# Performance work log

Hardware: AMD Instinct MI355X
Metric: run time of the kernel (lower is better)

The kernel has to match this reference:

```python
import math
import jax, jax.numpy as jnp
from jax import lax
import numpy as np

DT = 1.0 / 252.0  # dt_anos (dt_dias=1)

def _mlp(x, W1, b1, W2, b2, W3, b3):
    h = jax.nn.gelu(x @ W1 + b1, approximate=False)
    h = jax.nn.gelu(h @ W2 + b2, approximate=False)
    return h @ W3 + b3

def setup_inputs() -> dict:
    key = jax.random.key(0)
    ks = jax.random.split(key, 20)
    B, T = 64, 256
    d_ctx, d_h = 64 * 3, 128
    d_in = d_ctx + 2  # [r_mean, t_norm, ctx]
    def lin(k, din, dout):
        return jax.random.normal(k, (din, dout), dtype=jnp.float32) / np.sqrt(din)
    inp = {
        "X": jax.random.normal(ks[0], (B, T, 2), dtype=jnp.float32),
        "r_ultimo": jax.random.uniform(ks[1], (B,), dtype=jnp.float32) * 0.1,
        "maturidades": jnp.array([0.25, 0.5, 1.0, 2.0, 3.0, 5.0, 10.0], dtype=jnp.float32),
        "Wp": lin(ks[2], 2, 64), "bp": jnp.zeros((64,), jnp.float32),
        "ln_g": jnp.ones((64,), jnp.float32), "ln_b": jnp.zeros((64,), jnp.float32),
        "mu_W1": lin(ks[3], d_in, d_h), "mu_b1": jnp.zeros((d_h,), jnp.float32),
        "mu_W2": lin(ks[4], d_h, d_h), "mu_b2": jnp.zeros((d_h,), jnp.float32),
        "mu_W3": lin(ks[5], d_h, 1), "mu_b3": jnp.zeros((1,), jnp.float32),
        "si_W1": lin(ks[6], d_in, d_h), "si_b1": jnp.zeros((d_h,), jnp.float32),
        "si_W2": lin(ks[7], d_h, d_h), "si_b2": jnp.zeros((d_h,), jnp.float32),
        "si_W3": lin(ks[8], d_h, 1), "si_b3": jnp.zeros((1,), jnp.float32),
    }
    return inp

def _forward(n_steps, X, r_ultimo, maturidades, Wp, bp, ln_g, ln_b,
             mu_W1, mu_b1, mu_W2, mu_b2, mu_W3, mu_b3,
             si_W1, si_b1, si_W2, si_b2, si_W3, si_b3, Q=256):
    B = X.shape[0]
    # --- AgregadorContexto: LN(tanh(Linear(X))), mean/std(unbiased)/last ---
    H = jnp.tanh(X @ Wp + bp)                       # (B,T,64)
    m = H.mean(-1, keepdims=True)
    v = ((H - m) ** 2).mean(-1, keepdims=True)
    H = (H - m) / jnp.sqrt(v + 1e-5) * ln_g + ln_b
    ctx = jnp.concatenate([H.mean(1), H.std(1, ddof=1), H[:, -1, :]], axis=1)  # (B,192)
    # --- Euler-Maruyama MC of neural SDE ---
    max_T = maturidades.max()
    t_grid = jnp.linspace(0.0, 1.0, n_steps)
    keys = jax.random.split(jax.random.key(1), n_steps)
    sqrt_dt = math.sqrt(DT)
    def step(carry, inp):
        r, area = carry                              # (B,Q)
        t, k = inp
        x = jnp.concatenate(
            [r.mean(1, keepdims=True), jnp.broadcast_to(t, (B, 1)), ctx], axis=1)  # (B,194)
        mu = _mlp(x, mu_W1, mu_b1, mu_W2, mu_b2, mu_W3, mu_b3)[:, 0]
        si = jax.nn.softplus(_mlp(x, si_W1, si_b1, si_W2, si_b2, si_W3, si_b3)[:, 0]) + 1e-5
        dW = jax.random.normal(k, r.shape, dtype=r.dtype) * sqrt_dt
        r = r + mu[:, None] * DT + si[:, None] * dW
        area = area + r * DT
        return (r, area), None
    r0 = jnp.tile(r_ultimo[:, None], (1, Q))
    (r, area), _ = lax.scan(step, (r0, jnp.zeros((B, Q), X.dtype)), (t_grid, keys))
    frac = maturidades / (max_T + 1e-12)             # (Tm,)
    integrais = area.mean(1)[:, None] * frac[None, :]  # (B,Tm)
    return integrais / (maturidades[None, :] + 1e-12)

def reference(X, r_ultimo, maturidades, Wp, bp, ln_g, ln_b,
              mu_W1, mu_b1, mu_W2, mu_b2, mu_W3, mu_b3,
              si_W1, si_b1, si_W2, si_b2, si_W3, si_b3):
    max_T = float(np.asarray(maturidades).max())
    n_steps = max(2, int(math.ceil(max_T / DT)))     # 2520 for 10y
    return _forward(n_steps, X, r_ultimo, maturidades, Wp, bp, ln_g, ln_b,
                    mu_W1, mu_b1, mu_W2, mu_b2, mu_W3, mu_b3,
                    si_W1, si_b1, si_W2, si_b2, si_W3, si_b3)
```

## Files before the change

### kernel.cpp

```cpp
#include <hip/hip_runtime.h>
#include <stdint.h>


#define NSTEPS 2520
#define NB 64
#define NT 256
#define NQ 256
#define NMAT 7
#define NBODY 40
#define MWPAD 2560

typedef uint32_t u32x4 __attribute__((ext_vector_type(4)));
typedef float f32x4 __attribute__((ext_vector_type(4)));

__device__ __forceinline__ uint32_t rotl32(uint32_t v, int n) {
  return __builtin_amdgcn_alignbit(v, v, (uint32_t)(32 - n));
}

__device__ __forceinline__ void tf2x32(uint32_t k0, uint32_t k1,
                                       uint32_t x0, uint32_t x1,
                                       uint32_t& o0, uint32_t& o1) {
  const uint32_t k2 = k0 ^ k1 ^ 0x1BD11BDAu;
  x0 += k0; x1 += k1;
#define R4(a,b,c,d) \
  x0 += x1; x1 = rotl32(x1,(a)); x1 ^= x0; \
  x0 += x1; x1 = rotl32(x1,(b)); x1 ^= x0; \
  x0 += x1; x1 = rotl32(x1,(c)); x1 ^= x0; \
  x0 += x1; x1 = rotl32(x1,(d)); x1 ^= x0;
  R4(13,15,26,6)  x0 += k1; x1 += k2 + 1u;
  R4(17,29,16,24) x0 += k2; x1 += k0 + 2u;
  R4(13,15,26,6)  x0 += k0; x1 += k1 + 3u;
  R4(17,29,16,24) x0 += k1; x1 += k2 + 4u;
  R4(13,15,26,6)  x0 += k2; x1 += k0 + 5u;
  o0 = x0; o1 = x1;
}

__device__ __forceinline__ float fast_rcp(float q) {
  float r = __builtin_amdgcn_rcpf(q);
  r = __builtin_fmaf(r, __builtin_fmaf(-q, r, 1.0f), r);
  return r;
}

__device__ __forceinline__ float eigen_tanh(float a_x) {
  float x = fminf(fmaxf(a_x, -7.90531110763549805f), 7.90531110763549805f);
  float x2 = x * x;
  float p = __builtin_fmaf(x2, -2.76076847742355e-16f, 2.00018790482477e-13f);
  p = __builtin_fmaf(x2, p, -8.60467152213735e-11f);
  p = __builtin_fmaf(x2, p, 5.12229709037114e-08f);
  p = __builtin_fmaf(x2, p, 1.48572235717979e-05f);
  p = __builtin_fmaf(x2, p, 6.37261928875436e-04f);
  p = __builtin_fmaf(x2, p, 4.89352455891786e-03f);
  p = x * p;
  float q = __builtin_fmaf(x2, 1.19825839466702e-06f, 1.18534705686654e-04f);
  q = __builtin_fmaf(x2, q, 2.26843463243900e-03f);
  q = __builtin_fmaf(x2, q, 4.89352518554385e-03f);
  float rr = p / q;
  return (fabsf(a_x) < 0.0004f) ? a_x : rr;
}

__device__ __forceinline__ float eigen_erf_fast(float a_x) {
  float x = fminf(fmaxf(a_x, -4.0f), 4.0f);
  float x2 = x * x;
  float p = __builtin_fmaf(x2, -2.72614225801306e-10f, 2.77068142495902e-08f);
  p = __builtin_fmaf(x2, p, -2.10102402082508e-06f);
  p = __builtin_fmaf(x2, p, -5.69250639462346e-05f);
  p = __builtin_fmaf(x2, p, -7.34990630326855e-04f);
  p = __builtin_fmaf(x2, p, -2.95459980854025e-03f);
  p = __builtin_fmaf(x2, p, -1.60960333262415e-02f);
  p = x * p;
  float q = __builtin_fmaf(x2, -1.45660718464996e-05f, -2.13374055278905e-04f);
  q = __builtin_fmaf(x2, q, -1.68282697438203e-03f);
  q = __builtin_fmaf(x2, q, -7.37332916720468e-03f);
  q = __builtin_fmaf(x2, q, -1.42647390514189e-02f);
  return p * fast_rcp(q);
}

__device__ __forceinline__ uint16_t f32_to_f16bits(float x) {
  _Float16 hv = (_Float16)x;
  return __builtin_bit_cast(uint16_t, hv);
}

__device__ __forceinline__ uint32_t pack_f16x2(float lo, float hi) {
  return (uint32_t)f32_to_f16bits(lo) | ((uint32_t)f32_to_f16bits(hi) << 16);
}

template <int CTRL, int RMASK>
__device__ __forceinline__ float dpp_add(float v) {
  int x = __builtin_amdgcn_update_dpp(0, __float_as_int(v), CTRL, RMASK, 0xf, true);
  return v + __int_as_float(x);
}

__device__ __forceinline__ float dpp_reduce63(float p) {
  p = dpp_add<0x111, 0xf>(p);
  p = dpp_add<0x112, 0xf>(p);
  p = dpp_add<0x114, 0xf>(p);
  p = dpp_add<0x118, 0xf>(p);
  p = dpp_add<0x142, 0xa>(p);
  p = dpp_add<0x143, 0xc>(p);
  return p;
}

template <int CTRL, int RMASK>
__device__ __forceinline__ float dpp_mov(float v, float old) {
  int x = __builtin_amdgcn_update_dpp(__float_as_int(old), __float_as_int(v),
                                      CTRL, RMASK, 0xf, false);
  return __int_as_float(x);
}

__device__ __forceinline__ float readlane_f(float v, int l) {
  return __int_as_float(__builtin_amdgcn_readlane(__float_as_int(v), l));
}

#define DTF  0.00396825396825396826f
#define SQDT 0.06299407883487120442f
#define TSTEP (1.0f / 2519.0f)
#define TSC      64.0f
#define TSC_INV  0.015625f
#define TSC_T    1024.0f
#define TSCT_INV 0.0009765625f
#define INV_SQRT2 0.7071067811865475f
#define PHI_C     0.3989422804014327f
#define NEG_LN2  -0.69314718055994530942f
#define LG2_W5   -7.2134752044448170368f
#define NRM_C    0.08908708063747479f

__global__ __launch_bounds__(256)
void vasicek_phase1_meandw(float* __restrict__ ws) {
  const int tid = threadIdx.x;
  const int lane = tid & 63;
  const int wv = tid >> 6;
  const int wid = blockIdx.x * 4 + wv;
  const int b = wid / NSTEPS;
  const int s = wid - b * NSTEPS;

  uint32_t kA, kB;
  tf2x32(0u, 1u, 0u, (uint32_t)s, kA, kB);
  const uint32_t k2 = kA ^ kB ^ 0x1BD11BDAu;
  const uint32_t x1base = (uint32_t)(b * NQ + lane) + kB;

  const float MINVAL = -0.999999940395355224609375f;
  float sum = 0.f;
#pragma unroll
  for (int i = 0; i < 4; ++i) {
    uint32_t x0 = kA, x1 = x1base + (uint32_t)(i * 64);
    R4(13,15,26,6)  x0 += kB; x1 += k2 + 1u;
    R4(17,29,16,24) x0 += k2; x1 += kA + 2u;
    R4(13,15,26,6)  x0 += kA; x1 += kB + 3u;
    R4(17,29,16,24) x0 += kB; x1 += k2 + 4u;
    R4(13,15,26,6)  x0 += k2; x1 += kA + 5u;
    const uint32_t bits = x0 ^ x1;

    uint32_t fb = (bits >> 9) | 0x3F800000u;
    float u = __builtin_fmaf(__uint_as_float(fb) - 1.0f, 2.0f, MINVAL);
    u = fmaxf(u, MINVAL);
    float omsq = __builtin_fmaf(u, -u, 1.0f);
    float lg = __builtin_amdgcn_logf(omsq);
    float wc = __builtin_fmaf(lg, NEG_LN2, -2.5f);
    float p = 2.81022636e-08f;
    p = __builtin_fmaf(p, wc, 3.43273939e-07f);
    p = __builtin_fmaf(p, wc, -3.5233877e-06f);
    p = __builtin_fmaf(p, wc, -4.39150654e-06f);
    p = __builtin_fmaf(p, wc, 0.00021858087f);
    p = __builtin_fmaf(p, wc, -0.00125372503f);
    p = __builtin_fmaf(p, wc, -0.00417768164f);
    p = __builtin_fmaf(p, wc, 0.246640727f);
    p = __builtin_fmaf(p, wc, 1.50140941f);
    if (__ballot(lg <= LG2_W5)) {
      float w = lg * NEG_LN2;
      float wsr = sqrtf(w) - 3.0f;
      float pr = -0.000200214257f;
      pr = __builtin_fmaf(pr, wsr, 0.000100950558f);
      pr = __builtin_fmaf(pr, wsr, 0.00134934322f);
      pr = __builtin_fmaf(pr, wsr, -0.00367342844f);
      pr = __builtin_fmaf(pr, wsr, 0.00573950773f);
      pr = __builtin_fmaf(pr, wsr, -0.0076224613f);
      pr = __builtin_fmaf(pr, wsr, 0.00943887047f);
      pr = __builtin_fmaf(pr, wsr, 1.00167406f);
      pr = __builtin_fmaf(pr, wsr, 2.83297682f);
      p = (lg <= LG2_W5) ? pr : p;
    }
    sum = __builtin_fmaf(p * u, NRM_C, sum);
  }
  sum += __shfl_xor(sum, 32, 64); sum += __shfl_xor(sum, 16, 64);
  sum += __shfl_xor(sum, 8, 64);  sum += __shfl_xor(sum, 4, 64);
  sum += __shfl_xor(sum, 2, 64);  sum += __shfl_xor(sum, 1, 64);
  if (lane == 0) ws[b * NSTEPS + s] = sum * (1.0f / 256.0f);
}

#define BDECL(T, C) u32x4 b_##T##_##C;
#define BINIT(T, C) { \
  const int col_ = 16 * (4 * half + (C)) + n; \
  const int r0_ = 16 * (T) + 4 * q; \
  b_##T##_##C = (u32x4){ \
    pack_f16x2(W2src[(r0_ + 0) * 128 + col_], W2src[(r0_ + 64) * 128 + col_]), \
    pack_f16x2(W2src[(r0_ + 1) * 128 + col_], W2src[(r0_ + 65) * 128 + col_]), \
    pack_f16x2(W2src[(r0_ + 2) * 128 + col_], W2src[(r0_ + 66) * 128 + col_]), \
    pack_f16x2(W2src[(r0_ + 3) * 128 + col_], W2src[(r0_ + 67) * 128 + col_])}; \
  asm volatile("" : "+a"(b_##T##_##C));  \
}
#define MFMA1(ACC, AF, BF) \
  asm("v_mfma_f32_16x16x32_f16 %0, %1, %2, %0" : "+v"(ACC) : "v"(AF), "a"(BF));

#define STAGE3M(TV, SLOT, A_) { \
  float pre_ = __builtin_fmaf((TV), w11, __builtin_fmaf((A_), w10, c1)); \
  float e_ = eigen_erf_fast(pre_ * INV_SQRT2); \
  float cg_ = (e_ + 1.0f) * 0.5f; \
  float v_ = pre_ * cg_; \
  float ph_ = PHI_C * __expf(-0.5f * pre_ * pre_); \
  float gp_ = __builtin_fmaf(pre_, ph_, cg_); \
  ((uint16_t*)&h1x[SLOT][mlp][0][0])[2 * lane + half] = f32_to_f16bits(v_); \
  ((uint16_t*)&h1x[SLOT][mlp][1][0])[2 * lane + half] = f32_to_f16bits(gp_ * w10S); \
  ((uint16_t*)&h1x[SLOT][mlp][2][0])[2 * lane + half] = f32_to_f16bits(gp_ * w11T); \
}

__global__
__attribute__((amdgpu_flat_work_group_size(256, 256)))
__attribute__((amdgpu_waves_per_eu(1, 1)))
void vasicek_phase2_scan(
    const float* __restrict__ X, const float* __restrict__ r_ult,
    const float* __restrict__ mats,
    const float* __restrict__ Wp, const float* __restrict__ bp,
    const float* __restrict__ ln_g, const float* __restrict__ ln_b,
    const float* __restrict__ muW1, const float* __restrict__ mub1,
    const float* __restrict__ muW2, const float* __restrict__ mub2,
    const float* __restrict__ muW3, const float* __restrict__ mub3,
    const float* __restrict__ siW1, const float* __restrict__ sib1,
    const float* __restrict__ siW2, const float* __restrict__ sib2,
    const float* __restrict__ siW3, const float* __restrict__ sib3,
    const float* __restrict__ ws, float* __restrict__ out) {
  __shared__ __align__(16) uint32_t h1x[2][2][4][68];
  __shared__ __align__(16) float meanw[MWPAD];
  __shared__ float part[256];
  __shared__ float mbuf[64];
  __shared__ float ctx_lds[192];
  __shared__ __align__(16) float msum[2][4][4];

  const int t = threadIdx.x;
  const int b = blockIdx.x;
  const int lane = t & 63;
  const int wv = t >> 6;

  for (int i = t; i < MWPAD; i += 256)
    meanw[i] = i < NSTEPS ? ws[b * NSTEPS + i] : 0.f;

  float h[64];
  {
    float x0 = X[(b * NT + t) * 2 + 0];
    float x1 = X[(b * NT + t) * 2 + 1];
    float s = 0.f;
#pragma unroll
    for (int c = 0; c < 64; ++c) {
      float pre = __builtin_fmaf(x1, Wp[64 + c], x0 * Wp[c]) + bp[c];
      h[c] = eigen_tanh(pre);
      s += h[c];
    }
    float m = s * 0.015625f;
    float vs = 0.f;
#pragma unroll
    for (int c = 0; c < 64; ++c) { float d = h[c] - m; vs = __builtin_fmaf(d, d, vs); }
    float den = sqrtf(vs * 0.015625f + 1e-5f);
#pragma unroll
    for (int c = 0; c < 64; ++c)
      h[c] = ((h[c] - m) / den) * ln_g[c] + ln_b[c];
  }
#pragma unroll
  for (int c = 0; c < 64; ++c) {
    float v = h[c];
    v += __shfl_xor(v, 32, 64); v += __shfl_xor(v, 16, 64);
    v += __shfl_xor(v, 8, 64);  v += __shfl_xor(v, 4, 64);
    v += __shfl_xor(v, 2, 64);  v += __shfl_xor(v, 1, 64);
    if (lane == 0) part[wv * 64 + c] = v;
  }
  __syncthreads();
  if (t < 64) {
    float m = ((part[t] + part[64 + t]) + (part[128 + t] + part[192 + t])) * (1.0f / 256.0f);
    mbuf[t] = m;
    ctx_lds[t] = m;
  }
  __syncthreads();
#pragma unroll
  for (int c = 0; c < 64; ++c) {
    float d = h[c] - mbuf[c];
    float v = d * d;
    v += __shfl_xor(v, 32, 64); v += __shfl_xor(v, 16, 64);
    v += __shfl_xor(v, 8, 64);  v += __shfl_xor(v, 4, 64);
    v += __shfl_xor(v, 2, 64);  v += __shfl_xor(v, 1, 64);
    if (lane == 0) part[wv * 64 + c] = v;
  }
  if (t == 255) {
#pragma unroll
    for (int c = 0; c < 64; ++c) ctx_lds[128 + c] = h[c];
  }
  __syncthreads();
  if (t < 64) {
    float vs = (part[t] + part[64 + t]) + (part[128 + t] + part[192 + t]);
    ctx_lds[64 + t] = sqrtf(vs / 255.0f);
  }
  __syncthreads();

  const int mlp = wv >> 1;
  const int half = wv & 1;
  const int jH = 64 * half + lane;
  const float* W1 = mlp == 0 ? muW1 : siW1;
  const float* W2src = mlp == 0 ? muW2 : siW2;
  float c1 = (mlp == 0 ? mub1 : sib1)[jH];
  for (int c = 0; c < 192; ++c) {
    const float cx = ctx_lds[c];
    c1 = __builtin_fmaf(cx, W1[(2 + c) * 128 + jH], c1);
  }
  const float w10 = W1[jH], w11 = W1[128 + jH];
  const float w10S = w10 * TSC;
  const float w11T = w11 * (TSTEP * TSC_T);
  const float b3mu = mub3[0], b3si = sib3[0];

  const int q = lane >> 4, n = lane & 15;

  const float* b2p = mlp == 0 ? mub2 : sib2;
  const float* w3p = mlp == 0 ? muW3 : siW3;
  const int colE = 64 * half + 16 * q + n;
  const float b2E = b2p[colE], w3E = w3p[colE];

  BDECL(0,0) BDECL(0,1) BDECL(0,2) BDECL(0,3)
  BDECL(1,0) BDECL(1,1) BDECL(1,2) BDECL(1,3)
  BDECL(2,0) BDECL(2,1) BDECL(2,2) BDECL(2,3)
  BDECL(3,0) BDECL(3,1) BDECL(3,2) BDECL(3,3)
  BINIT(0,0) BINIT(0,1) BINIT(0,2) BINIT(0,3)
  BINIT(1,0) BINIT(1,1) BINIT(1,2) BINIT(1,3)
  BINIT(2,0) BINIT(2,1) BINIT(2,2) BINIT(2,3)
  BINIT(3,0) BINIT(3,1) BINIT(3,2) BINIT(3,3)

  h1x[0][mlp][3][lane] = 0u; h1x[1][mlp][3][lane] = 0u;
  if (lane < 4) { h1x[0][mlp][3][64 + lane] = 0u; h1x[1][mlp][3][64 + lane] = 0u; }

  const u32x4* hq0 = ((const u32x4*)&h1x[0][mlp][0][0]) + 17 * (n & 3) + q;
  const u32x4* hq1 = ((const u32x4*)&h1x[1][mlp][0][0]) + 17 * (n & 3) + q;

  const float r0 = r_ult[b];
  float r_s = r0;
  float aNow = r0, aUpd = r0, aMid = r0;
  float area_p = 0.f;
  const int sj = lane;
  const float jj = (float)sj - 31.5f;

  STAGE3M(TSTEP * 31.5f, 0, r0)
  __syncthreads();

#pragma unroll 1
  for (int k = -1; k < NBODY; ++k) {
    const int sl = k & 1;
    const int so = sl ^ 1;

    f32x4 m0 = *(const f32x4*)&msum[sl][0][0];
    f32x4 m1 = *(const f32x4*)&msum[sl][1][0];
    f32x4 m2 = *(const f32x4*)&msum[sl][2][0];
    f32x4 m3 = *(const f32x4*)&msum[sl][3][0];
    const int u0 = k < 0 ? 0 : 64 * k;
    const float mwj = meanw[u0 + sj];
    const u32x4* hq = so ? hq1 : hq0;
    u32x4 af0 = hq[0], af1 = hq[4], af2 = hq[8], af3 = hq[12];

    f32x4 ac0 = {0,0,0,0}, ac1 = {0,0,0,0}, ac2 = {0,0,0,0}, ac3 = {0,0,0,0};
    MFMA1(ac0, af0, b_0_0) MFMA1(ac1, af0, b_0_1) MFMA1(ac2, af0, b_0_2) MFMA1(ac3, af0, b_0_3)
    MFMA1(ac0, af1, b_1_0) MFMA1(ac1, af1, b_1_1) MFMA1(ac2, af1, b_1_2) MFMA1(ac3, af1, b_1_3)
    MFMA1(ac0, af2, b_2_0) MFMA1(ac1, af2, b_2_1) MFMA1(ac2, af2, b_2_2) MFMA1(ac3, af2, b_2_3)
    MFMA1(ac0, af3, b_3_0) MFMA1(ac1, af3, b_3_1) MFMA1(ac2, af3, b_3_2) MFMA1(ac3, af3, b_3_3)

    STAGE3M(TSTEP * ((float)(64 * (k + 2)) + 31.5f), sl, aMid)

    {
      float MV = (m0[0] + m1[0]) + b3mu;
      float MR = (m0[1] + m1[1]) * TSC_INV;
      float MT = (m0[2] + m1[2]) * TSCT_INV;
      float ZV = (m2[0] + m3[0]) + b3si;
      float ZR = (m2[1] + m3[1]) * TSC_INV;
      float ZT = (m2[2] + m3[2]) * TSCT_INV;
      float e_ = __expf(-fabsf(ZV));
      float sp = fmaxf(ZV, 0.f) + __logf(1.0f + e_) + 1e-5f;
      float inv = fast_rcp(1.0f + e_);
      float sgm = ZV > 0.f ? inv : 1.0f - inv;
      float hcv = 0.5f * sgm * (1.0f - sgm);
      float dzt = jj * ZT;
      float sigj = __builtin_fmaf(2.0f * hcv, dzt, sgm);
      float spj  = __builtin_fmaf(__builtin_fmaf(hcv, dzt, sgm), dzt, sp);
      float sZR = sigj * ZR;
      float beta = __builtin_fmaf(sZR, mwj, __builtin_fmaf(MR, DTF, 1.0f));
      float am_ = __builtin_fmaf(jj, MT, __builtin_fmaf(-aNow, MR, MV));
      float as_ = __builtin_fmaf(-aNow, sZR, spj);
      float alpha = __builtin_fmaf(am_, DTF, as_ * mwj);
      float B = beta, A = alpha;
      {
        float Bs = dpp_mov<0x111, 0xf>(B, 1.0f), As = dpp_mov<0x111, 0xf>(A, 0.0f);
        A = __builtin_fmaf(B, As, A); B = B * Bs;
        Bs = dpp_mov<0x112, 0xf>(B, 1.0f); As = dpp_mov<0x112, 0xf>(A, 0.0f);
        A = __builtin_fmaf(B, As, A); B = B * Bs;
        Bs = dpp_mov<0x114, 0xf>(B, 1.0f); As = dpp_mov<0x114, 0xf>(A, 0.0f);
        A = __builtin_fmaf(B, As, A); B = B * Bs;
        Bs = dpp_mov<0x118, 0xf>(B, 1.0f); As = dpp_mov<0x118, 0xf>(A, 0.0f);
        A = __builtin_fmaf(B, As, A); B = B * Bs;
        Bs = dpp_mov<0x142, 0xa>(B, 1.0f); As = dpp_mov<0x142, 0xa>(A, 0.0f);
        A = __builtin_fmaf(B, As, A); B = B * Bs;
        Bs = dpp_mov<0x143, 0xc>(B, 1.0f); As = dpp_mov<0x143, 0xc>(A, 0.0f);
        A = __builtin_fmaf(B, As, A); B = B * Bs;
      }
      float rho = __builtin_fmaf(B, r_s, A);
      if (k >= 0) {
        float contrib = (64 * k + sj) < NSTEPS ? rho * DTF : 0.f;
        area_p += contrib;
        float rn = readlane_f(rho, 63);
        float aNew = __builtin_fmaf(MV, 160.5f * DTF, rn);
        r_s = rn;
        aNow = aUpd; aUpd = aMid; aMid = aNew;
      }
    }

    asm volatile("s_nop 7\n\ts_nop 7"
                 : "+v"(ac0), "+v"(ac1), "+v"(ac2), "+v"(ac3));

    {
      const f32x4 aq = q == 0 ? ac0 : q == 1 ? ac1 : q == 2 ? ac2 : ac3;
      float yv = aq[0] + b2E;
      float ytr = aq[1];
      float ytt = aq[2];
      float ev = eigen_erf_fast(yv * INV_SQRT2);
      float cv = (ev + 1.0f) * 0.5f;
      float pv = yv * cv * w3E;
      float phv = PHI_C * __expf(-0.5f * yv * yv);
      float g2p = __builtin_fmaf(yv, phv, cv) * w3E;
      float pr = g2p * ytr;
      float pt = g2p * ytt;
      pv = dpp_reduce63(pv);
      pr = dpp_reduce63(pr);
      pt = dpp_reduce63(pt);
      if (lane == 63) {
        *(f32x4*)&msum[so][wv][0] = (f32x4){pv, pr, pt, 0.f};
      }
    }
    __syncthreads();
  }

  float area = area_p;
  area += __shfl_xor(area, 1, 64);
  area += __shfl_xor(area, 2, 64);
  area += __shfl_xor(area, 4, 64);
  area += __shfl_xor(area, 8, 64);
  area += __shfl_xor(area, 16, 64);
  area += __shfl_xor(area, 32, 64);

  if (t < NMAT) {
    float mx = mats[0];
#pragma unroll
    for (int i = 1; i < NMAT; ++i) mx = fmaxf(mx, mats[i]);
    const float mm = mats[t];
    const float frac = mm / (mx + 1e-12f);
    out[b * NMAT + t] = (area * frac) / (mm + 1e-12f);
  }
}

extern "C" void kernel_launch(void* const* d_in, const int* in_sizes, int n_in,
                              void* d_out, int out_size, void* d_ws, size_t ws_size,
                              hipStream_t stream) {
  (void)in_sizes; (void)n_in; (void)ws_size; (void)out_size;
  const float* X      = (const float*)d_in[0];
  const float* r_ult  = (const float*)d_in[1];
  const float* mats   = (const float*)d_in[2];
  const float* Wp     = (const float*)d_in[3];
  const float* bp     = (const float*)d_in[4];
  const float* ln_g   = (const float*)d_in[5];
  const float* ln_b   = (const float*)d_in[6];
  const float* muW1   = (const float*)d_in[7];
  const float* mub1   = (const float*)d_in[8];
  const float* muW2   = (const float*)d_in[9];
  const float* mub2   = (const float*)d_in[10];
  const float* muW3   = (const float*)d_in[11];
  const float* mub3   = (const float*)d_in[12];
  const float* siW1   = (const float*)d_in[13];
  const float* sib1   = (const float*)d_in[14];
  const float* siW2   = (const float*)d_in[15];
  const float* sib2   = (const float*)d_in[16];
  const float* siW3   = (const float*)d_in[17];
  const float* sib3   = (const float*)d_in[18];
  float* ws = (float*)d_ws;

  hipLaunchKernelGGL(vasicek_phase1_meandw,
                     dim3(NB * NSTEPS / 4), dim3(256), 0, stream, ws);
  hipLaunchKernelGGL(vasicek_phase2_scan,
                     dim3(NB), dim3(256), 0, stream,
                     X, r_ult, mats, Wp, bp, ln_g, ln_b,
                     muW1, mub1, muW2, mub2, muW3, mub3,
                     siW1, sib1, siW2, sib2, siW3, sib3,
                     ws, (float*)d_out);
}
```

Before: 270.3 us.

## Pack two batch rows per 512-thread workgroup in the scan kernel

The scan kernel now handles two batch elements per workgroup, using 8 waves and half as many blocks. All shared-memory buffers gain a per-batch dimension, and the waves_per_eu(1,1) hint is dropped. The aim is to put two independent, latency-bound scan chains on each CU so their MFMA, LDS and sync latencies overlap. In exchange, the per-step barrier now spans both chains, only half the CUs are used, and each wave has a smaller register budget, which may cause spills of the AGPR-resident weights.

Result: slower. 288.0 us (+6.6%).

```diff
diff --git a/kernel.cpp b/kernel.cpp
--- a/kernel.cpp
+++ b/kernel.cpp
@@ -208,14 +208,13 @@
   float v_ = pre_ * cg_; \
   float ph_ = PHI_C * __expf(-0.5f * pre_ * pre_); \
   float gp_ = __builtin_fmaf(pre_, ph_, cg_); \
-  ((uint16_t*)&h1x[SLOT][mlp][0][0])[2 * lane + half] = f32_to_f16bits(v_); \
-  ((uint16_t*)&h1x[SLOT][mlp][1][0])[2 * lane + half] = f32_to_f16bits(gp_ * w10S); \
-  ((uint16_t*)&h1x[SLOT][mlp][2][0])[2 * lane + half] = f32_to_f16bits(gp_ * w11T); \
+  ((uint16_t*)&h1x[SLOT][pb][mlp][0][0])[2 * lane + half] = f32_to_f16bits(v_); \
+  ((uint16_t*)&h1x[SLOT][pb][mlp][1][0])[2 * lane + half] = f32_to_f16bits(gp_ * w10S); \
+  ((uint16_t*)&h1x[SLOT][pb][mlp][2][0])[2 * lane + half] = f32_to_f16bits(gp_ * w11T); \
 }
 
 __global__
-__attribute__((amdgpu_flat_work_group_size(256, 256)))
-__attribute__((amdgpu_waves_per_eu(1, 1)))
+__attribute__((amdgpu_flat_work_group_size(512, 512)))
 void vasicek_phase2_scan(
     const float* __restrict__ X, const float* __restrict__ r_ult,
     const float* __restrict__ mats,
@@ -228,25 +227,30 @@
     const float* __restrict__ siW2, const float* __restrict__ sib2,
     const float* __restrict__ siW3, const float* __restrict__ sib3,
     const float* __restrict__ ws, float* __restrict__ out) {
-  __shared__ __align__(16) uint32_t h1x[2][2][4][68];
-  __shared__ __align__(16) float meanw[MWPAD];
-  __shared__ float part[256];
-  __shared__ float mbuf[64];
-  __shared__ float ctx_lds[192];
-  __shared__ __align__(16) float msum[2][4][4];
+  __shared__ __align__(16) uint32_t h1x[2][2][2][4][68];
+  __shared__ __align__(16) float meanw[2][MWPAD];
+  __shared__ float part[2][256];
+  __shared__ float mbuf[2][64];
+  __shared__ float ctx_lds[2][192];
+  __shared__ __align__(16) float msum[2][2][4][4];
 
   const int t = threadIdx.x;
-  const int b = blockIdx.x;
   const int lane = t & 63;
   const int wv = t >> 6;
-
-  for (int i = t; i < MWPAD; i += 256)
-    meanw[i] = i < NSTEPS ? ws[b * NSTEPS + i] : 0.f;
+  const int pb = wv >> 2;
+  const int wvr = wv & 3;
+  const int tt = t & 255;
+  const int b = blockIdx.x * 2 + pb;
+
+  for (int i = t; i < 2 * MWPAD; i += 512) {
+    int pbi = i / MWPAD, si = i - pbi * MWPAD;
+    meanw[pbi][si] = si < NSTEPS ? ws[(blockIdx.x * 2 + pbi) * NSTEPS + si] : 0.f;
+  }
 
   float h[64];
   {
-    float x0 = X[(b * NT + t) * 2 + 0];
-    float x1 = X[(b * NT + t) * 2 + 1];
+    float x0 = X[(b * NT + tt) * 2 + 0];
+    float x1 = X[(b * NT + tt) * 2 + 1];
     float s = 0.f;
 #pragma unroll
     for (int c = 0; c < 64; ++c) {
@@ -269,43 +273,45 @@
     v += __shfl_xor(v, 32, 64); v += __shfl_xor(v, 16, 64);
     v += __shfl_xor(v, 8, 64);  v += __shfl_xor(v, 4, 64);
     v += __shfl_xor(v, 2, 64);  v += __shfl_xor(v, 1, 64);
-    if (lane == 0) part[wv * 64 + c] = v;
+    if (lane == 0) part[pb][wvr * 64 + c] = v;
   }
   __syncthreads();
-  if (t < 64) {
-    float m = ((part[t] + part[64 + t]) + (part[128 + t] + part[192 + t])) * (1.0f / 256.0f);
-    mbuf[t] = m;
-    ctx_lds[t] = m;
+  if (tt < 64) {
+    float m = ((part[pb][tt] + part[pb][64 + tt]) +
+               (part[pb][128 + tt] + part[pb][192 + tt])) * (1.0f / 256.0f);
+    mbuf[pb][tt] = m;
+    ctx_lds[pb][tt] = m;
   }
   __syncthreads();
 #pragma unroll
   for (int c = 0; c < 64; ++c) {
-    float d = h[c] - mbuf[c];
+    float d = h[c] - mbuf[pb][c];
     float v = d * d;
     v += __shfl_xor(v, 32, 64); v += __shfl_xor(v, 16, 64);
     v += __shfl_xor(v, 8, 64);  v += __shfl_xor(v, 4, 64);
     v += __shfl_xor(v, 2, 64);  v += __shfl_xor(v, 1, 64);
-    if (lane == 0) part[wv * 64 + c] = v;
-  }
-  if (t == 255) {
-#pragma unroll
-    for (int c = 0; c < 64; ++c) ctx_lds[128 + c] = h[c];
+    if (lane == 0) part[pb][wvr * 64 + c] = v;
+  }
+  if (tt == 255) {
+#pragma unroll
+    for (int c = 0; c < 64; ++c) ctx_lds[pb][128 + c] = h[c];
   }
   __syncthreads();
-  if (t < 64) {
-    float vs = (part[t] + part[64 + t]) + (part[128 + t] + part[192 + t]);
-    ctx_lds[64 + t] = sqrtf(vs / 255.0f);
+  if (tt < 64) {
+    float vs = (part[pb][tt] + part[pb][64 + tt]) +
+               (part[pb][128 + tt] + part[pb][192 + tt]);
+    ctx_lds[pb][64 + tt] = sqrtf(vs / 255.0f);
   }
   __syncthreads();
 
-  const int mlp = wv >> 1;
-  const int half = wv & 1;
+  const int mlp = wvr >> 1;
+  const int half = wvr & 1;
   const int jH = 64 * half + lane;
   const float* W1 = mlp == 0 ? muW1 : siW1;
   const float* W2src = mlp == 0 ? muW2 : siW2;
   float c1 = (mlp == 0 ? mub1 : sib1)[jH];
   for (int c = 0; c < 192; ++c) {
-    const float cx = ctx_lds[c];
+    const float cx = ctx_lds[pb][c];
     c1 = __builtin_fmaf(cx, W1[(2 + c) * 128 + jH], c1);
   }
   const float w10 = W1[jH], w11 = W1[128 + jH];
@@ -329,11 +335,13 @@
   BINIT(2,0) BINIT(2,1) BINIT(2,2) BINIT(2,3)
   BINIT(3,0) BINIT(3,1) BINIT(3,2) BINIT(3,3)
 
-  h1x[0][mlp][3][lane] = 0u; h1x[1][mlp][3][lane] = 0u;
-  if (lane < 4) { h1x[0][mlp][3][64 + lane] = 0u; h1x[1][mlp][3][64 + lane] = 0u; }
-
-  const u32x4* hq0 = ((const u32x4*)&h1x[0][mlp][0][0]) + 17 * (n & 3) + q;
-  const u32x4* hq1 = ((const u32x4*)&h1x[1][mlp][0][0]) + 17 * (n & 3) + q;
+  h1x[0][pb][mlp][3][lane] = 0u; h1x[1][pb][mlp][3][lane] = 0u;
+  if (lane < 4) {
+    h1x[0][pb][mlp][3][64 + lane] = 0u; h1x[1][pb][mlp][3][64 + lane] = 0u;
+  }
+
+  const u32x4* hq0 = ((const u32x4*)&h1x[0][pb][mlp][0][0]) + 17 * (n & 3) + q;
+  const u32x4* hq1 = ((const u32x4*)&h1x[1][pb][mlp][0][0]) + 17 * (n & 3) + q;
 
   const float r0 = r_ult[b];
   float r_s = r0;
@@ -350,12 +358,12 @@
     const int sl = k & 1;
     const int so = sl ^ 1;
 
-    f32x4 m0 = *(const f32x4*)&msum[sl][0][0];
-    f32x4 m1 = *(const f32x4*)&msum[sl][1][0];
-    f32x4 m2 = *(const f32x4*)&msum[sl][2][0];
-    f32x4 m3 = *(const f32x4*)&msum[sl][3][0];
+    f32x4 m0 = *(const f32x4*)&msum[sl][pb][0][0];
+    f32x4 m1 = *(const f32x4*)&msum[sl][pb][1][0];
+    f32x4 m2 = *(const f32x4*)&msum[sl][pb][2][0];
+    f32x4 m3 = *(const f32x4*)&msum[sl][pb][3][0];
     const int u0 = k < 0 ? 0 : 64 * k;
-    const float mwj = meanw[u0 + sj];
+    const float mwj = meanw[pb][u0 + sj];
     const u32x4* hq = so ? hq1 : hq0;
     u32x4 af0 = hq[0], af1 = hq[4], af2 = hq[8], af3 = hq[12];
 
@@ -432,7 +440,7 @@
       pr = dpp_reduce63(pr);
       pt = dpp_reduce63(pt);
       if (lane == 63) {
-        *(f32x4*)&msum[so][wv][0] = (f32x4){pv, pr, pt, 0.f};
+        *(f32x4*)&msum[so][pb][wvr][0] = (f32x4){pv, pr, pt, 0.f};
       }
     }
     __syncthreads();
@@ -446,13 +454,13 @@
   area += __shfl_xor(area, 16, 64);
   area += __shfl_xor(area, 32, 64);
 
-  if (t < NMAT) {
+  if (wvr == 0 && lane < NMAT) {
     float mx = mats[0];
 #pragma unroll
     for (int i = 1; i < NMAT; ++i) mx = fmaxf(mx, mats[i]);
-    const float mm = mats[t];
+    const float mm = mats[lane];
     const float frac = mm / (mx + 1e-12f);
-    out[b * NMAT + t] = (area * frac) / (mm + 1e-12f);
+    out[b * NMAT + lane] = (area * frac) / (mm + 1e-12f);
   }
 }
 
@@ -484,7 +492,7 @@
   hipLaunchKernelGGL(vasicek_phase1_meandw,
                      dim3(NB * NSTEPS / 4), dim3(256), 0, stream, ws);
   hipLaunchKernelGGL(vasicek_phase2_scan,
-                     dim3(NB), dim3(256), 0, stream,
+                     dim3(NB / 2), dim3(512), 0, stream,
                      X, r_ult, mats, Wp, bp, ln_g, ln_b,
                      muW1, mub1, muW2, mub2, muW3, mub3,
                      siW1, sib1, siW2, sib2, siW3, sib3,
```

## Replace serial pipelined chunk scan with two-pass parallel chunk linearization

Applied to the files above, without the earlier changes.

The serial 41-step loop, which needed a block barrier every step, is replaced by a two-pass scheme. Each wave first evaluates the MLP for all 40 chunks at a fixed anchor state: the initial rate in pass 0, and the pass-0 chunk-start states in pass 1. The per-chunk affine scans are then split across waves, and one wave does a cross-chunk scan to get chunk start states. This removes per-step barriers and cross-wave dependency, at the cost of duplicating layer-1 work per wave, running the MLP twice, and changing which states the linearization uses.

Measured after the change: 288.7 us. 1.07x slower.

```diff
diff --git a/kernel.cpp b/kernel.cpp
--- a/kernel.cpp
+++ b/kernel.cpp
@@ -105,6 +105,22 @@
   int x = __builtin_amdgcn_update_dpp(__float_as_int(old), __float_as_int(v),
                                       CTRL, RMASK, 0xf, false);
   return __int_as_float(x);
+}
+
+__device__ __forceinline__ void affine_scan64(float& B, float& A) {
+  float Bs, As;
+  Bs = dpp_mov<0x111, 0xf>(B, 1.0f); As = dpp_mov<0x111, 0xf>(A, 0.0f);
+  A = __builtin_fmaf(B, As, A); B = B * Bs;
+  Bs = dpp_mov<0x112, 0xf>(B, 1.0f); As = dpp_mov<0x112, 0xf>(A, 0.0f);
+  A = __builtin_fmaf(B, As, A); B = B * Bs;
+  Bs = dpp_mov<0x114, 0xf>(B, 1.0f); As = dpp_mov<0x114, 0xf>(A, 0.0f);
+  A = __builtin_fmaf(B, As, A); B = B * Bs;
+  Bs = dpp_mov<0x118, 0xf>(B, 1.0f); As = dpp_mov<0x118, 0xf>(A, 0.0f);
+  A = __builtin_fmaf(B, As, A); B = B * Bs;
+  Bs = dpp_mov<0x142, 0xa>(B, 1.0f); As = dpp_mov<0x142, 0xa>(A, 0.0f);
+  A = __builtin_fmaf(B, As, A); B = B * Bs;
+  Bs = dpp_mov<0x143, 0xc>(B, 1.0f); As = dpp_mov<0x143, 0xc>(A, 0.0f);
+  A = __builtin_fmaf(B, As, A); B = B * Bs;
 }
 
 __device__ __forceinline__ float readlane_f(float v, int l) {
@@ -201,21 +217,8 @@
 #define MFMA1(ACC, AF, BF) \
   asm("v_mfma_f32_16x16x32_f16 %0, %1, %2, %0" : "+v"(ACC) : "v"(AF), "a"(BF));
 
-#define STAGE3M(TV, SLOT, A_) { \
-  float pre_ = __builtin_fmaf((TV), w11, __builtin_fmaf((A_), w10, c1)); \
-  float e_ = eigen_erf_fast(pre_ * INV_SQRT2); \
-  float cg_ = (e_ + 1.0f) * 0.5f; \
-  float v_ = pre_ * cg_; \
-  float ph_ = PHI_C * __expf(-0.5f * pre_ * pre_); \
-  float gp_ = __builtin_fmaf(pre_, ph_, cg_); \
-  ((uint16_t*)&h1x[SLOT][mlp][0][0])[2 * lane + half] = f32_to_f16bits(v_); \
-  ((uint16_t*)&h1x[SLOT][mlp][1][0])[2 * lane + half] = f32_to_f16bits(gp_ * w10S); \
-  ((uint16_t*)&h1x[SLOT][mlp][2][0])[2 * lane + half] = f32_to_f16bits(gp_ * w11T); \
-}
-
 __global__
 __attribute__((amdgpu_flat_work_group_size(256, 256)))
-__attribute__((amdgpu_waves_per_eu(1, 1)))
 void vasicek_phase2_scan(
     const float* __restrict__ X, const float* __restrict__ r_ult,
     const float* __restrict__ mats,
@@ -228,12 +231,17 @@
     const float* __restrict__ siW2, const float* __restrict__ sib2,
     const float* __restrict__ siW3, const float* __restrict__ sib3,
     const float* __restrict__ ws, float* __restrict__ out) {
-  __shared__ __align__(16) uint32_t h1x[2][2][4][68];
+  __shared__ __align__(16) uint32_t h1p[2][4][4][68];
   __shared__ __align__(16) float meanw[MWPAD];
   __shared__ float part[256];
   __shared__ float mbuf[64];
   __shared__ float ctx_lds[192];
-  __shared__ __align__(16) float msum[2][4][4];
+  __shared__ float c1buf[2][128];
+  __shared__ __align__(16) float msum_l[NBODY][4][4];
+  __shared__ __align__(8)  float part_lds[NBODY][64][2];
+  __shared__ __align__(8)  float bsc[NBODY][2];
+  __shared__ float re_lds[NBODY];
+  __shared__ float areas[4];
 
   const int t = threadIdx.x;
   const int b = blockIdx.x;
@@ -300,21 +308,31 @@
 
   const int mlp = wv >> 1;
   const int half = wv & 1;
-  const int jH = 64 * half + lane;
+  {
+    const int jH = 64 * half + lane;
+    const float* W1c = mlp == 0 ? muW1 : siW1;
+    float c1 = (mlp == 0 ? mub1 : sib1)[jH];
+    for (int c = 0; c < 192; ++c) {
+      const float cx = ctx_lds[c];
+      c1 = __builtin_fmaf(cx, W1c[(2 + c) * 128 + jH], c1);
+    }
+    c1buf[mlp][jH] = c1;
+  }
+  h1p[0][wv][3][lane] = 0u; h1p[1][wv][3][lane] = 0u;
+  if (lane < 4) { h1p[0][wv][3][64 + lane] = 0u; h1p[1][wv][3][64 + lane] = 0u; }
+  __syncthreads();
+
   const float* W1 = mlp == 0 ? muW1 : siW1;
   const float* W2src = mlp == 0 ? muW2 : siW2;
-  float c1 = (mlp == 0 ? mub1 : sib1)[jH];
-  for (int c = 0; c < 192; ++c) {
-    const float cx = ctx_lds[c];
-    c1 = __builtin_fmaf(cx, W1[(2 + c) * 128 + jH], c1);
-  }
-  const float w10 = W1[jH], w11 = W1[128 + jH];
-  const float w10S = w10 * TSC;
-  const float w11T = w11 * (TSTEP * TSC_T);
+  const float c1a = c1buf[mlp][lane];
+  const float c1b = c1buf[mlp][64 + lane];
+  const float w10a = W1[lane],        w11a = W1[128 + lane];
+  const float w10b = W1[64 + lane],   w11b = W1[192 + lane];
+  const float w10aS = w10a * TSC,     w10bS = w10b * TSC;
+  const float w11aT = w11a * (TSTEP * TSC_T), w11bT = w11b * (TSTEP * TSC_T);
   const float b3mu = mub3[0], b3si = sib3[0];
 
   const int q = lane >> 4, n = lane & 15;
-
   const float* b2p = mlp == 0 ? mub2 : sib2;
   const float* w3p = mlp == 0 ? muW3 : siW3;
   const int colE = 64 * half + 16 * q + n;
@@ -329,45 +347,64 @@
   BINIT(2,0) BINIT(2,1) BINIT(2,2) BINIT(2,3)
   BINIT(3,0) BINIT(3,1) BINIT(3,2) BINIT(3,3)
 
-  h1x[0][mlp][3][lane] = 0u; h1x[1][mlp][3][lane] = 0u;
-  if (lane < 4) { h1x[0][mlp][3][64 + lane] = 0u; h1x[1][mlp][3][64 + lane] = 0u; }
-
-  const u32x4* hq0 = ((const u32x4*)&h1x[0][mlp][0][0]) + 17 * (n & 3) + q;
-  const u32x4* hq1 = ((const u32x4*)&h1x[1][mlp][0][0]) + 17 * (n & 3) + q;
-
   const float r0 = r_ult[b];
-  float r_s = r0;
-  float aNow = r0, aUpd = r0, aMid = r0;
-  float area_p = 0.f;
-  const int sj = lane;
-  const float jj = (float)sj - 31.5f;
-
-  STAGE3M(TSTEP * 31.5f, 0, r0)
-  __syncthreads();
+  const float jj = (float)lane - 31.5f;
 
 #pragma unroll 1
-  for (int k = -1; k < NBODY; ++k) {
-    const int sl = k & 1;
-    const int so = sl ^ 1;
-
-    f32x4 m0 = *(const f32x4*)&msum[sl][0][0];
-    f32x4 m1 = *(const f32x4*)&msum[sl][1][0];
-    f32x4 m2 = *(const f32x4*)&msum[sl][2][0];
-    f32x4 m3 = *(const f32x4*)&msum[sl][3][0];
-    const int u0 = k < 0 ? 0 : 64 * k;
-    const float mwj = meanw[u0 + sj];
-    const u32x4* hq = so ? hq1 : hq0;
-    u32x4 af0 = hq[0], af1 = hq[4], af2 = hq[8], af3 = hq[12];
-
-    f32x4 ac0 = {0,0,0,0}, ac1 = {0,0,0,0}, ac2 = {0,0,0,0}, ac3 = {0,0,0,0};
-    MFMA1(ac0, af0, b_0_0) MFMA1(ac1, af0, b_0_1) MFMA1(ac2, af0, b_0_2) MFMA1(ac3, af0, b_0_3)
-    MFMA1(ac0, af1, b_1_0) MFMA1(ac1, af1, b_1_1) MFMA1(ac2, af1, b_1_2) MFMA1(ac3, af1, b_1_3)
-    MFMA1(ac0, af2, b_2_0) MFMA1(ac1, af2, b_2_1) MFMA1(ac2, af2, b_2_2) MFMA1(ac3, af2, b_2_3)
-    MFMA1(ac0, af3, b_3_0) MFMA1(ac1, af3, b_3_1) MFMA1(ac2, af3, b_3_2) MFMA1(ac3, af3, b_3_3)
-
-    STAGE3M(TSTEP * ((float)(64 * (k + 2)) + 31.5f), sl, aMid)
-
-    {
+  for (int pass = 0; pass < 2; ++pass) {
+#pragma unroll 2
+    for (int k = 0; k < NBODY; ++k) {
+      const float aK = pass == 0 ? r0 : re_lds[k];
+      const float tvk = TSTEP * ((float)(64 * k) + 31.5f);
+      const int hb = k & 1;
+      float prea = __builtin_fmaf(tvk, w11a, __builtin_fmaf(aK, w10a, c1a));
+      float preb = __builtin_fmaf(tvk, w11b, __builtin_fmaf(aK, w10b, c1b));
+      float ea = eigen_erf_fast(prea * INV_SQRT2);
+      float ca = (ea + 1.0f) * 0.5f;
+      float va = prea * ca;
+      float pha = PHI_C * __expf(-0.5f * prea * prea);
+      float gpa = __builtin_fmaf(prea, pha, ca);
+      float eb = eigen_erf_fast(preb * INV_SQRT2);
+      float cb = (eb + 1.0f) * 0.5f;
+      float vb = preb * cb;
+      float phb = PHI_C * __expf(-0.5f * preb * preb);
+      float gpb = __builtin_fmaf(preb, phb, cb);
+      h1p[hb][wv][0][lane] = pack_f16x2(va, vb);
+      h1p[hb][wv][1][lane] = pack_f16x2(gpa * w10aS, gpb * w10bS);
+      h1p[hb][wv][2][lane] = pack_f16x2(gpa * w11aT, gpb * w11bT);
+      const u32x4* hq = ((const u32x4*)&h1p[hb][wv][0][0]) + 17 * (n & 3) + q;
+      u32x4 af0 = hq[0], af1 = hq[4], af2 = hq[8], af3 = hq[12];
+      f32x4 ac0 = {0,0,0,0}, ac1 = {0,0,0,0}, ac2 = {0,0,0,0}, ac3 = {0,0,0,0};
+      MFMA1(ac0, af0, b_0_0) MFMA1(ac1, af0, b_0_1) MFMA1(ac2, af0, b_0_2) MFMA1(ac3, af0, b_0_3)
+      MFMA1(ac0, af1, b_1_0) MFMA1(ac1, af1, b_1_1) MFMA1(ac2, af1, b_1_2) MFMA1(ac3, af1, b_1_3)
+      MFMA1(ac0, af2, b_2_0) MFMA1(ac1, af2, b_2_1) MFMA1(ac2, af2, b_2_2) MFMA1(ac3, af2, b_2_3)
+      MFMA1(ac0, af3, b_3_0) MFMA1(ac1, af3, b_3_1) MFMA1(ac2, af3, b_3_2) MFMA1(ac3, af3, b_3_3)
+      asm volatile("s_nop 7\n\ts_nop 7"
+                   : "+v"(ac0), "+v"(ac1), "+v"(ac2), "+v"(ac3));
+      const f32x4 aq = q == 0 ? ac0 : q == 1 ? ac1 : q == 2 ? ac2 : ac3;
+      float yv = aq[0] + b2E;
+      float ev = eigen_erf_fast(yv * INV_SQRT2);
+      float cv = (ev + 1.0f) * 0.5f;
+      float pv = yv * cv * w3E;
+      float phv = PHI_C * __expf(-0.5f * yv * yv);
+      float g2p = __builtin_fmaf(yv, phv, cv) * w3E;
+      float pr = g2p * aq[1];
+      float pt = g2p * aq[2];
+      pv = dpp_reduce63(pv);
+      pr = dpp_reduce63(pr);
+      pt = dpp_reduce63(pt);
+      if (lane == 63) *(f32x4*)&msum_l[k][wv][0] = (f32x4){pv, pr, pt, 0.f};
+    }
+    __syncthreads();
+
+    for (int kk = 0; kk < 10; ++kk) {
+      const int k = 10 * wv + kk;
+      f32x4 m0 = *(const f32x4*)&msum_l[k][0][0];
+      f32x4 m1 = *(const f32x4*)&msum_l[k][1][0];
+      f32x4 m2 = *(const f32x4*)&msum_l[k][2][0];
+      f32x4 m3 = *(const f32x4*)&msum_l[k][3][0];
+      const float aK = pass == 0 ? r0 : re_lds[k];
+      const float mwj = meanw[64 * k + lane];
       float MV = (m0[0] + m1[0]) + b3mu;
       float MR = (m0[1] + m1[1]) * TSC_INV;
       float MT = (m0[2] + m1[2]) * TSCT_INV;
@@ -384,69 +421,45 @@
       float spj  = __builtin_fmaf(__builtin_fmaf(hcv, dzt, sgm), dzt, sp);
       float sZR = sigj * ZR;
       float beta = __builtin_fmaf(sZR, mwj, __builtin_fmaf(MR, DTF, 1.0f));
-      float am_ = __builtin_fmaf(jj, MT, __builtin_fmaf(-aNow, MR, MV));
-      float as_ = __builtin_fmaf(-aNow, sZR, spj);
+      float am_ = __builtin_fmaf(jj, MT, __builtin_fmaf(-aK, MR, MV));
+      float as_ = __builtin_fmaf(-aK, sZR, spj);
       float alpha = __builtin_fmaf(am_, DTF, as_ * mwj);
       float B = beta, A = alpha;
-      {
-        float Bs = dpp_mov<0x111, 0xf>(B, 1.0f), As = dpp_mov<0x111, 0xf>(A, 0.0f);
-        A = __builtin_fmaf(B, As, A); B = B * Bs;
-        Bs = dpp_mov<0x112, 0xf>(B, 1.0f); As = dpp_mov<0x112, 0xf>(A, 0.0f);
-        A = __builtin_fmaf(B, As, A); B = B * Bs;
-        Bs = dpp_mov<0x114, 0xf>(B, 1.0f); As = dpp_mov<0x114, 0xf>(A, 0.0f);
-        A = __builtin_fmaf(B, As, A); B = B * Bs;
-        Bs = dpp_mov<0x118, 0xf>(B, 1.0f); As = dpp_mov<0x118, 0xf>(A, 0.0f);
-        A = __builtin_fmaf(B, As, A); B = B * Bs;
-        Bs = dpp_mov<0x142, 0xa>(B, 1.0f); As = dpp_mov<0x142, 0xa>(A, 0.0f);
-        A = __builtin_fmaf(B, As, A); B = B * Bs;
-        Bs = dpp_mov<0x143, 0xc>(B, 1.0f); As = dpp_mov<0x143, 0xc>(A, 0.0f);
-        A = __builtin_fmaf(B, As, A); B = B * Bs;
-      }
-      float rho = __builtin_fmaf(B, r_s, A);
-      if (k >= 0) {
-        float contrib = (64 * k + sj) < NSTEPS ? rho * DTF : 0.f;
-        area_p += contrib;
-        float rn = readlane_f(rho, 63);
-        float aNew = __builtin_fmaf(MV, 160.5f * DTF, rn);
-        r_s = rn;
-        aNow = aUpd; aUpd = aMid; aMid = aNew;
-      }
-    }
-
-    asm volatile("s_nop 7\n\ts_nop 7"
-                 : "+v"(ac0), "+v"(ac1), "+v"(ac2), "+v"(ac3));
-
-    {
-      const f32x4 aq = q == 0 ? ac0 : q == 1 ? ac1 : q == 2 ? ac2 : ac3;
-      float yv = aq[0] + b2E;
-      float ytr = aq[1];
-      float ytt = aq[2];
-      float ev = eigen_erf_fast(yv * INV_SQRT2);
-      float cv = (ev + 1.0f) * 0.5f;
-      float pv = yv * cv * w3E;
-      float phv = PHI_C * __expf(-0.5f * yv * yv);
-      float g2p = __builtin_fmaf(yv, phv, cv) * w3E;
-      float pr = g2p * ytr;
-      float pt = g2p * ytt;
-      pv = dpp_reduce63(pv);
-      pr = dpp_reduce63(pr);
-      pt = dpp_reduce63(pt);
-      if (lane == 63) {
-        *(f32x4*)&msum[so][wv][0] = (f32x4){pv, pr, pt, 0.f};
-      }
+      affine_scan64(B, A);
+      part_lds[k][lane][0] = B;
+      part_lds[k][lane][1] = A;
+      if (lane == 63) { bsc[k][0] = B; bsc[k][1] = A; }
     }
     __syncthreads();
-  }
-
-  float area = area_p;
-  area += __shfl_xor(area, 1, 64);
-  area += __shfl_xor(area, 2, 64);
-  area += __shfl_xor(area, 4, 64);
-  area += __shfl_xor(area, 8, 64);
-  area += __shfl_xor(area, 16, 64);
-  area += __shfl_xor(area, 32, 64);
+
+    if (wv == 0) {
+      float B = 1.0f, A = 0.0f;
+      if (lane < NBODY) { B = bsc[lane][0]; A = bsc[lane][1]; }
+      affine_scan64(B, A);
+      float st = __builtin_fmaf(B, r0, A);
+      part[lane] = st;
+      float re = lane == 0 ? r0 : part[lane - 1];
+      if (lane < NBODY) re_lds[lane] = re;
+    }
+    __syncthreads();
+  }
+
+  {
+    float ap = 0.f;
+    for (int kk = 0; kk < 10; ++kk) {
+      const int k = 10 * wv + kk;
+      float B = part_lds[k][lane][0];
+      float A = part_lds[k][lane][1];
+      float rho = __builtin_fmaf(B, re_lds[k], A);
+      if (64 * k + lane < NSTEPS) ap = __builtin_fmaf(rho, DTF, ap);
+    }
+    ap = dpp_reduce63(ap);
+    if (lane == 63) areas[wv] = ap;
+  }
+  __syncthreads();
 
   if (t < NMAT) {
+    float area = (areas[0] + areas[1]) + (areas[2] + areas[3]);
     float mx = mats[0];
 #pragma unroll
     for (int i = 1; i < NMAT; ++i) mx = fmaxf(mx, mats[i]);
```
